# Kernel optimization log

Hardware: AMD Instinct MI355X
Metric: run time of the kernel (lower is better)

Reference implementation:

```python
import jax, jax.numpy as jnp
import numpy as np

N = 50000   # nodes
E = 800000  # edges
IN = 128
H = 256
OUT = 10
G = 128     # graphs in batch


def _uniform(key, shape, fan_in):
    bound = 1.0 / np.sqrt(fan_in)
    return jax.random.uniform(key, shape, jnp.float32, -bound, bound)


def setup_inputs() -> dict:
    key = jax.random.key(0)
    ks = jax.random.split(key, 12)
    x = jax.random.normal(ks[0], (N, IN), jnp.float32)
    edge_index = jax.random.randint(ks[1], (2, E), 0, N, dtype=jnp.int64)
    edge_weight = jax.random.uniform(ks[2], (E,), jnp.float32)
    batch = jnp.sort(jax.random.randint(ks[3], (N,), 0, G, dtype=jnp.int64))
    # GCNConv weights (bias=False)
    W0 = _uniform(ks[4], (IN, H), IN)
    W1 = _uniform(ks[5], (H, H), H)
    W2 = _uniform(ks[6], (H, H), H)
    # MLP head: [H, H, OUT]
    Wm1 = _uniform(ks[7], (H, H), H)
    bm1 = _uniform(ks[8], (H,), H)
    Wm2 = _uniform(ks[9], (H, OUT), H)
    bm2 = _uniform(ks[10], (OUT,), H)
    return dict(x=x, edge_index=edge_index, edge_weight=edge_weight, batch=batch,
                W0=W0, W1=W1, W2=W2, Wm1=Wm1, bm1=bm1, Wm2=Wm2, bm2=bm2)


def _gcn_conv(h, W, row, col, dinv_sqrt):
    """GCNConv with self-loops and symmetric deg^-1/2 normalization, bias=False.
    Self-loop contribution handled analytically (norm = dinv_sqrt[i]^2)."""
    hw = h @ W                                        # [N, H]
    norm = dinv_sqrt[row] * dinv_sqrt[col]            # [E]
    msg = hw[row] * norm[:, None]                     # [E, H] gather-scale
    agg = jax.ops.segment_sum(msg, col, num_segments=N)  # scatter-add at targets
    return agg + (dinv_sqrt * dinv_sqrt)[:, None] * hw    # add self-loop term


def reference(x, edge_index, edge_weight, batch, W0, W1, W2, Wm1, bm1, Wm2, bm2):
    row, col = edge_index[0], edge_index[1]
    # degree including self-loop (edge_weight is ignored, as in the source)
    deg = jax.ops.segment_sum(jnp.ones((E,), x.dtype), col, num_segments=N) + 1.0
    dinv_sqrt = jax.lax.rsqrt(deg)
    h = x
    for W in (W0, W1, W2):
        h = jax.nn.relu(_gcn_conv(h, W, row, col, dinv_sqrt))
    # global mean pool over graphs
    counts = jax.ops.segment_sum(jnp.ones((N,), h.dtype), batch, num_segments=G)
    pooled = jax.ops.segment_sum(h, batch, num_segments=G) / jnp.maximum(counts, 1.0)[:, None]
    # MLP head (dropout inactive at inference)
    hmid = jax.nn.relu(pooled @ Wm1 + bm1)
    last = hmid @ Wm2 + bm2
    return jax.nn.log_softmax(last, axis=-1), jax.nn.sigmoid(last), last
```

## Files before the change

### kernel.cpp

```cpp
#include <hip/hip_runtime.h>
#include <math.h>

#define N_NODES 50000
#define N_PAD   50048
#define N_EDGES 800000
#define CSR_CAP 1200000
#define IN_F 128
#define H_F 256
#define OUT_F 10
#define N_G 128
#define NCHUNKS 196

typedef __attribute__((ext_vector_type(4))) float f32x4;
typedef __attribute__((ext_vector_type(2))) float f32x2;
typedef unsigned char u8;

__device__ inline f32x2 fp8x2_f32_lo(unsigned int v) {
    return __builtin_amdgcn_cvt_pk_f32_fp8(v, false);
}
__device__ inline f32x2 fp8x2_f32_hi(unsigned int v) {
    return __builtin_amdgcn_cvt_pk_f32_fp8(v, true);
}
__device__ inline unsigned int f32_fp8x2_lo(float a, float b, unsigned int old) {
    return __builtin_amdgcn_cvt_pk_fp8_f32(a, b, old, false);
}
__device__ inline unsigned int f32_fp8x2_hi(float a, float b, unsigned int old) {
    return __builtin_amdgcn_cvt_pk_fp8_f32(a, b, old, true);
}
__device__ inline u8 f32_fp8(float a) {
    return (u8)(f32_fp8x2_lo(a, a, 0u) & 0xff);
}
__device__ inline ushort f2bf(float x) {
    union { float f; unsigned int u; } v; v.f = x;
    unsigned int r = v.u + 0x7fff + ((v.u >> 16) & 1);
    return (ushort)(r >> 16);
}
__device__ inline float bf2f(ushort u) {
    union { unsigned int u; float f; } v; v.u = ((unsigned int)u) << 16; return v.f;
}

__device__ inline void gl2lds16(const void* g, void* l) {
    __builtin_amdgcn_global_load_lds(
        (const __attribute__((address_space(1))) unsigned int*)g,
        (__attribute__((address_space(3))) unsigned int*)l,
        16, 0, 0);
}

#define PREP_HIST 782
#define PREP_X   (PREP_HIST + 6250)
#define PREP_T0  (PREP_X + 128)
#define PREP_T1  (PREP_T0 + 256)
#define PREP_T2  (PREP_T1 + 256)
#define PREP_GS  (PREP_T2 + NCHUNKS)

__global__ __launch_bounds__(256) void prep_kernel(
    const int* __restrict__ col, int* __restrict__ counts,
    int* __restrict__ rank,
    const float* __restrict__ x, u8* __restrict__ xb,
    const float* __restrict__ W0, u8* __restrict__ W0t,
    const float* __restrict__ W1, u8* __restrict__ W1t,
    const float* __restrict__ W2, u8* __restrict__ W2t,
    const int* __restrict__ batch, int* __restrict__ gstart) {
    int b = blockIdx.x;
    int tid = threadIdx.x;
    if (b < PREP_HIST) {
        int base = b * 1024 + tid;
        int c[4];
        #pragma unroll
        for (int u = 0; u < 4; ++u) {
            int e = base + u * 256;
            c[u] = (e < N_EDGES) ? col[e] : -1;
        }
        int rk[4];
        #pragma unroll
        for (int u = 0; u < 4; ++u)
            if (c[u] >= 0) rk[u] = atomicAdd(&counts[c[u]], 1);
        #pragma unroll
        for (int u = 0; u < 4; ++u)
            if (c[u] >= 0) rank[base + u * 256] = rk[u];
    } else if (b < PREP_X) {
        int i = (b - PREP_HIST) * 256 + tid;
        float4 v = *(const float4*)(x + (size_t)i * 4);
        unsigned int p = f32_fp8x2_lo(v.x, v.y, 0u);
        p = f32_fp8x2_hi(v.z, v.w, p);
        *(unsigned int*)(xb + (size_t)i * 4) = p;
    } else if (b < PREP_T0) {
        int idx = (b - PREP_X) * 256 + tid;
        int k = idx >> 8, nn = idx & 255;
        W0t[nn * IN_F + k] = f32_fp8(W0[idx]);
    } else if (b < PREP_T1) {
        int idx = (b - PREP_T0) * 256 + tid;
        int k = idx >> 8, nn = idx & 255;
        W1t[nn * H_F + k] = f32_fp8(W1[idx]);
    } else if (b < PREP_T2) {
        int idx = (b - PREP_T1) * 256 + tid;
        int k = idx >> 8, nn = idx & 255;
        W2t[nn * H_F + k] = f32_fp8(W2[idx]);
    } else {
        int i = (b - PREP_T2) * 256 + tid;
        if (i >= N_NODES) return;
        int bb = batch[i];
        if (i == 0) {
            for (int g = 0; g <= bb; ++g) gstart[g] = 0;
        } else {
            int p = batch[i - 1];
            if (p != bb) { for (int g = p + 1; g <= bb; ++g) gstart[g] = i; }
        }
        if (i == N_NODES - 1) {
            for (int g = bb + 1; g <= N_G; ++g) gstart[g] = N_NODES;
        }
    }
}

__global__ __launch_bounds__(256) void chunk_reduce(const int* __restrict__ counts,
                                                    int* __restrict__ csum, int n) {
    int i = blockIdx.x * 256 + threadIdx.x;
    int v = (i < n) ? ((counts[i] + 7) & ~7) : 0;
    #pragma unroll
    for (int off = 32; off; off >>= 1) v += __shfl_down(v, off);
    __shared__ int ws[4];
    if ((threadIdx.x & 63) == 0) ws[threadIdx.x >> 6] = v;
    __syncthreads();
    if (threadIdx.x == 0) csum[blockIdx.x] = ws[0] + ws[1] + ws[2] + ws[3];
}

__global__ __launch_bounds__(256) void scan_dinv_kernel(const int* __restrict__ counts,
                                                        const int* __restrict__ csum,
                                                        int* __restrict__ offsets,
                                                        float* __restrict__ dinv,
                                                        unsigned int* __restrict__ csr_ew,
                                                        int n) {
    int tid = threadIdx.x;
    int lane = tid & 63, wid = tid >> 6;
    int cv = (tid < NCHUNKS) ? csum[tid] : 0;
    int xc = cv;
    #pragma unroll
    for (int off = 1; off < 64; off <<= 1) {
        int t = __shfl_up(xc, off);
        if (lane >= off) xc += t;
    }
    __shared__ int cw[4], cpre[4];
    __shared__ int cexcl[257];
    if (lane == 63) cw[wid] = xc;
    __syncthreads();
    if (tid == 0) { int s = 0; for (int k = 0; k < 4; ++k) { cpre[k] = s; s += cw[k]; } }
    __syncthreads();
    cexcl[tid] = cpre[wid] + xc - cv;
    if (tid == 255) cexcl[256] = cpre[3] + cw[3];
    __syncthreads();
    int base = cexcl[blockIdx.x];
    int i = blockIdx.x * 256 + tid;
    int v = (i < n) ? counts[i] : 0;
    int pv = (v + 7) & ~7;
    int x = pv;
    #pragma unroll
    for (int off = 1; off < 64; off <<= 1) {
        int t = __shfl_up(x, off);
        if (lane >= off) x += t;
    }
    __shared__ int wsum[4], wpre[4];
    if (lane == 63) wsum[wid] = x;
    __syncthreads();
    if (tid == 0) { int s = 0; for (int k = 0; k < 4; ++k) { wpre[k] = s; s += wsum[k]; } }
    __syncthreads();
    if (i < n) {
        int o = base + wpre[wid] + x - pv;
        offsets[i] = o;
        dinv[i] = rsqrtf((float)(v + 1));
        for (int z = v; z < pv; ++z) csr_ew[o + z] = 0u;
    }
    if (blockIdx.x == 0 && tid == 0) offsets[n] = cexcl[NCHUNKS];
}

__global__ __launch_bounds__(256) void fill_csr_kernel(const int* __restrict__ row,
                                                       const int* __restrict__ col,
                                                       const int* __restrict__ offsets,
                                                       const int* __restrict__ rank,
                                                       const float* __restrict__ dinv,
                                                       unsigned int* __restrict__ csr_ew) {
    int e0 = blockIdx.x * 512 + threadIdx.x;
    int e1 = e0 + 256;
    int c0 = -1, c1 = -1, r0 = 0, r1 = 0, k0 = 0, k1 = 0;
    if (e0 < N_EDGES) { c0 = col[e0]; r0 = row[e0]; k0 = rank[e0]; }
    if (e1 < N_EDGES) { c1 = col[e1]; r1 = row[e1]; k1 = rank[e1]; }
    float dc0 = 0.f, dr0 = 0.f, dc1 = 0.f, dr1 = 0.f;
    if (c0 >= 0) { dc0 = dinv[c0]; dr0 = dinv[r0]; }
    if (c1 >= 0) { dc1 = dinv[c1]; dr1 = dinv[r1]; }
    if (c0 >= 0)
        csr_ew[offsets[c0] + k0] = (unsigned int)r0 | ((unsigned int)f2bf(dc0 * dr0) << 16);
    if (c1 >= 0)
        csr_ew[offsets[c1] + k1] = (unsigned int)r1 | ((unsigned int)f2bf(dc1 * dr1) << 16);
}

template <int K, bool RELU>
__global__ __launch_bounds__(256) void gemm_fp8(const u8* __restrict__ A,
                                                const u8* __restrict__ Bt,
                                                u8* __restrict__ C) {
    __shared__ u8 As[4 * 4096];
    __shared__ u8 Bs[4 * 4096];
    int tid = threadIdx.x;
    int lane = tid & 63;
    int w = tid >> 6;
    int wm = w & 1, wn = w >> 1;
    int l16 = lane & 15, quad = lane >> 4;
    int row0 = blockIdx.x * 128;
    int col0 = blockIdx.y * 128;
    f32x4 acc[4][4] = {};

    int sr = tid >> 1;
    int sh = (tid & 1) * 16;
    const u8* ga = A + (size_t)(row0 + sr) * K + sh;
    const u8* gb = Bt + (size_t)(col0 + sr) * K + sh;

    #pragma unroll
    for (int k0 = 0; k0 < K; k0 += 128) {
        if (k0) __syncthreads();
        #pragma unroll
        for (int q = 0; q < 4; ++q) {
            gl2lds16(ga + k0 + q * 32, As + q * 4096 + w * 1024);
            gl2lds16(gb + k0 + q * 32, Bs + q * 4096 + w * 1024);
        }
        __syncthreads();
        #pragma unroll
        for (int h = 0; h < 4; ++h) {
            long af[4], bfr[4];
            #pragma unroll
            for (int i = 0; i < 4; ++i)
                af[i] = *(const long*)&As[h * 4096 + (wm * 64 + i * 16 + l16) * 32 + quad * 8];
            #pragma unroll
            for (int j = 0; j < 4; ++j)
                bfr[j] = *(const long*)&Bs[h * 4096 + (wn * 64 + j * 16 + l16) * 32 + quad * 8];
            #pragma unroll
            for (int i = 0; i < 4; ++i)
                #pragma unroll
                for (int j = 0; j < 4; ++j)
                    acc[i][j] = __builtin_amdgcn_mfma_f32_16x16x32_fp8_fp8(af[i], bfr[j], acc[i][j], 0, 0, 0);
        }
    }
    #pragma unroll
    for (int i = 0; i < 4; ++i) {
        int rowb = row0 + wm * 64 + i * 16 + quad * 4;
        #pragma unroll
        for (int r = 0; r < 4; ++r) {
            int grow = rowb + r;
            #pragma unroll
            for (int j = 0; j < 4; ++j) {
                int gcol = col0 + wn * 64 + j * 16 + l16;
                float v = acc[i][j][r];
                if (RELU) v = fmaxf(v, 0.f);
                C[(size_t)grow * H_F + gcol] = f32_fp8(v);
            }
        }
    }
}

__global__ __launch_bounds__(256) void aggregate128(const u8* __restrict__ hw,
                                                    const float* __restrict__ dinv,
                                                    const int* __restrict__ offsets,
                                                    const unsigned int* __restrict__ csr_ew,
                                                    u8* __restrict__ hout) {
    int w = threadIdx.x >> 6;
    int lane = threadIdx.x & 63;
    int i = blockIdx.x * 4 + w;
    if (i >= N_NODES) return;
    float di = dinv[i];
    const u8* base = hw + (size_t)lane * 2;
    unsigned int su = *(const unsigned short*)(base + (size_t)i * IN_F);
    f32x2 sv = fp8x2_f32_lo(su);
    float s = di * di;
    float a0 = s * sv.x, a1 = s * sv.y;
    int t = __builtin_amdgcn_readfirstlane(offsets[i]);
    int end = __builtin_amdgcn_readfirstlane(offsets[i + 1]);
    if (t < end) {
        uint4 eA = *(const uint4*)(csr_ew + t);
        uint4 eB = *(const uint4*)(csr_ew + t + 4);
        for (; t < end; t += 8) {
            uint4 nA, nB;
            if (t + 8 < end) {
                nA = *(const uint4*)(csr_ew + t + 8);
                nB = *(const uint4*)(csr_ew + t + 12);
            }
            unsigned int e[8] = {eA.x, eA.y, eA.z, eA.w, eB.x, eB.y, eB.z, eB.w};
            unsigned int v[8];
            #pragma unroll
            for (int u = 0; u < 8; ++u)
                v[u] = *(const unsigned short*)(base + (size_t)(e[u] & 0xffff) * IN_F);
            #pragma unroll
            for (int u = 0; u < 8; ++u) {
                float wq = bf2f((ushort)(e[u] >> 16));
                f32x2 f = fp8x2_f32_lo(v[u]);
                a0 += wq * f.x; a1 += wq * f.y;
            }
            eA = nA; eB = nB;
        }
    }
    unsigned int o = f32_fp8x2_lo(a0, a1, 0u);
    *(unsigned short*)(hout + (size_t)i * IN_F + lane * 2) = (unsigned short)(o & 0xffff);
}

__global__ __launch_bounds__(256) void aggregate256(const u8* __restrict__ hw,
                                                    const float* __restrict__ dinv,
                                                    const int* __restrict__ offsets,
                                                    const unsigned int* __restrict__ csr_ew,
                                                    u8* __restrict__ hout) {
    int w = threadIdx.x >> 6;
    int lane = threadIdx.x & 63;
    int i = blockIdx.x * 4 + w;
    if (i >= N_NODES) return;
    float di = dinv[i];
    const u8* base = hw + (size_t)lane * 4;
    unsigned int su = *(const unsigned int*)(base + (size_t)i * H_F);
    f32x2 slo = fp8x2_f32_lo(su), shi = fp8x2_f32_hi(su);
    float s = di * di;
    float a0 = s * slo.x, a1 = s * slo.y, a2 = s * shi.x, a3 = s * shi.y;
    int t = __builtin_amdgcn_readfirstlane(offsets[i]);
    int end = __builtin_amdgcn_readfirstlane(offsets[i + 1]);
    if (t < end) {
        uint4 eA = *(const uint4*)(csr_ew + t);
        uint4 eB = *(const uint4*)(csr_ew + t + 4);
        for (; t < end; t += 8) {
            uint4 nA, nB;
            if (t + 8 < end) {
                nA = *(const uint4*)(csr_ew + t + 8);
                nB = *(const uint4*)(csr_ew + t + 12);
            }
            unsigned int e[8] = {eA.x, eA.y, eA.z, eA.w, eB.x, eB.y, eB.z, eB.w};
            unsigned int v[8];
            #pragma unroll
            for (int u = 0; u < 8; ++u)
                v[u] = *(const unsigned int*)(base + (size_t)(e[u] & 0xffff) * H_F);
            #pragma unroll
            for (int u = 0; u < 8; ++u) {
                float wq = bf2f((ushort)(e[u] >> 16));
                f32x2 lo = fp8x2_f32_lo(v[u]), hi = fp8x2_f32_hi(v[u]);
                a0 += wq * lo.x; a1 += wq * lo.y;
                a2 += wq * hi.x; a3 += wq * hi.y;
            }
            eA = nA; eB = nB;
        }
    }
    unsigned int o = f32_fp8x2_lo(fmaxf(a0, 0.f), fmaxf(a1, 0.f), 0u);
    o = f32_fp8x2_hi(fmaxf(a2, 0.f), fmaxf(a3, 0.f), o);
    *(unsigned int*)(hout + (size_t)i * H_F + lane * 4) = o;
}

__global__ __launch_bounds__(1024) void pool_mlp_kernel(const u8* __restrict__ h,
                                                        const int* __restrict__ gstart,
                                                        const float* __restrict__ Wm1,
                                                        const float* __restrict__ bm1,
                                                        const float* __restrict__ Wm2,
                                                        const float* __restrict__ bm2,
                                                        float* __restrict__ out) {
    __shared__ float sm[16][H_F];
    __shared__ float p[H_F];
    __shared__ float hmid[H_F];
    __shared__ float lastv[OUT_F];
    __shared__ float stats[2];
    int g = blockIdx.x;
    int s = gstart[g], e = gstart[g + 1];
    int w = threadIdx.x >> 6;
    int lane = threadIdx.x & 63;
    float a0 = 0.f, a1 = 0.f, a2 = 0.f, a3 = 0.f;
    for (int i = s + w; i < e; i += 16) {
        unsigned int v = *(const unsigned int*)(h + (size_t)i * H_F + lane * 4);
        f32x2 lo = fp8x2_f32_lo(v), hi = fp8x2_f32_hi(v);
        a0 += lo.x; a1 += lo.y; a2 += hi.x; a3 += hi.y;
    }
    *(f32x4*)&sm[w][lane * 4] = (f32x4){a0, a1, a2, a3};
    __syncthreads();
    int j = threadIdx.x;
    int cnt = e - s;
    if (j < H_F) {
        float t = 0.f;
        #pragma unroll
        for (int k = 0; k < 16; ++k) t += sm[k][j];
        p[j] = t / (float)max(cnt, 1);
    }
    __syncthreads();
    if (j < H_F) {
        float acc = bm1[j];
        for (int k = 0; k < H_F; ++k) acc += p[k] * Wm1[k * H_F + j];
        hmid[j] = fmaxf(acc, 0.f);
    }
    __syncthreads();
    if (j < OUT_F) {
        float a = bm2[j];
        for (int k = 0; k < H_F; ++k) a += hmid[k] * Wm2[k * OUT_F + j];
        lastv[j] = a;
    }
    __syncthreads();
    if (j == 0) {
        float m = -1e30f;
        for (int o = 0; o < OUT_F; ++o) m = fmaxf(m, lastv[o]);
        float sxp = 0.f;
        for (int o = 0; o < OUT_F; ++o) sxp += expf(lastv[o] - m);
        stats[0] = m; stats[1] = logf(sxp);
    }
    __syncthreads();
    if (j < OUT_F) {
        float v = lastv[j];
        out[g * OUT_F + j] = v - stats[0] - stats[1];
        out[(size_t)N_G * OUT_F + g * OUT_F + j] = 1.f / (1.f + expf(-v));
        out[(size_t)2 * N_G * OUT_F + g * OUT_F + j] = v;
    }
}

extern "C" void kernel_launch(void* const* d_in, const int* in_sizes, int n_in,
                              void* d_out, int out_size, void* d_ws, size_t ws_size,
                              hipStream_t stream) {
    const float* x   = (const float*)d_in[0];
    const int* edge_index = (const int*)d_in[1];
    const int* batch = (const int*)d_in[3];
    const float* W0  = (const float*)d_in[4];
    const float* W1  = (const float*)d_in[5];
    const float* W2  = (const float*)d_in[6];
    const float* Wm1 = (const float*)d_in[7];
    const float* bm1 = (const float*)d_in[8];
    const float* Wm2 = (const float*)d_in[9];
    const float* bm2 = (const float*)d_in[10];
    float* out = (float*)d_out;

    char* ws = (char*)d_ws;
    size_t off = 0;
    auto alloc = [&](size_t bytes) -> void* {
        void* p = ws + off; off += (bytes + 255) & ~(size_t)255; return p;
    };
    u8* xb       = (u8*)alloc((size_t)N_PAD * IN_F);
    u8* bufA     = (u8*)alloc((size_t)N_PAD * H_F);
    u8* bufB     = (u8*)alloc((size_t)N_PAD * H_F);
    u8* t0       = (u8*)alloc((size_t)N_PAD * IN_F);
    u8* W0t      = (u8*)alloc((size_t)H_F * IN_F);
    u8* W1t      = (u8*)alloc((size_t)H_F * H_F);
    u8* W2t      = (u8*)alloc((size_t)H_F * H_F);
    float* dinv    = (float*)alloc((size_t)N_NODES * 4);
    int*   counts  = (int*)alloc((size_t)N_NODES * 4);
    int*   offsets = (int*)alloc((size_t)(N_NODES + 1) * 4);
    int*   rank    = (int*)alloc((size_t)N_EDGES * 4);
    unsigned int* csr_ew = (unsigned int*)alloc((size_t)CSR_CAP * 4);
    int*   csum    = (int*)alloc((size_t)256 * 4);
    int*   gstart  = (int*)alloc((size_t)(N_G + 1) * 4);

    const int* row = edge_index;
    const int* col = edge_index + N_EDGES;

    hipMemsetAsync(counts, 0, (size_t)N_NODES * 4, stream);

    prep_kernel<<<PREP_GS, 256, 0, stream>>>(col, counts, rank, x, xb, W0, W0t,
                                             W1, W1t, W2, W2t, batch, gstart);
    chunk_reduce<<<NCHUNKS, 256, 0, stream>>>(counts, csum, N_NODES);
    scan_dinv_kernel<<<NCHUNKS, 256, 0, stream>>>(counts, csum, offsets, dinv,
                                                  csr_ew, N_NODES);
    fill_csr_kernel<<<1563, 256, 0, stream>>>(row, col, offsets, rank, dinv, csr_ew);

    dim3 gg(N_PAD / 128, H_F / 128);
    int agg_blocks = (N_NODES + 3) / 4;
    aggregate128<<<agg_blocks, 256, 0, stream>>>(xb, dinv, offsets, csr_ew, t0);
    gemm_fp8<IN_F, true><<<gg, 256, 0, stream>>>(t0, W0t, bufA);
    gemm_fp8<H_F, false><<<gg, 256, 0, stream>>>(bufA, W1t, bufB);
    aggregate256<<<agg_blocks, 256, 0, stream>>>(bufB, dinv, offsets, csr_ew, bufA);
    gemm_fp8<H_F, false><<<gg, 256, 0, stream>>>(bufA, W2t, bufB);
    aggregate256<<<agg_blocks, 256, 0, stream>>>(bufB, dinv, offsets, csr_ew, bufA);

    pool_mlp_kernel<<<N_G, 1024, 0, stream>>>(bufA, gstart, Wm1, bm1, Wm2, bm2, out);
}
```

Baseline: 290.9 us.

## Replace global atomic degree histogram with partitioned LDS histograms

Swaps the global-atomic degree histogram for a 16x16 grid of blocks. Each block scans one edge partition and counts in LDS only the edges whose targets fall in its node range. Per-partition counts are summed in chunk_reduce and turned into per-partition exclusive offsets in scan_dinv, and fill_csr adds that offset to the LDS rank. This removes global atomic contention and the memset, but each edge is now read 16 times by the histogram blocks, and only 256 blocks each loop over 50k edges.

```diff
diff --git a/kernel.cpp b/kernel.cpp
--- a/kernel.cpp
+++ b/kernel.cpp
@@ -11,6 +11,11 @@
 #define N_G 128
 #define NCHUNKS 196
 
+#define P_PART 16
+#define R_RANGE 16
+#define PE (N_EDGES / P_PART)
+#define RN (N_NODES / R_RANGE)
+
 typedef __attribute__((ext_vector_type(4))) float f32x4;
 typedef __attribute__((ext_vector_type(2))) float f32x2;
 typedef unsigned char u8;
@@ -46,40 +51,43 @@
         16, 0, 0);
 }
 
-#define PREP_HIST 782
-#define PREP_X   (PREP_HIST + 6250)
+#define PREP_HB  (P_PART * R_RANGE)
+#define PREP_X   (PREP_HB + 6250)
 #define PREP_T0  (PREP_X + 128)
 #define PREP_T1  (PREP_T0 + 256)
 #define PREP_T2  (PREP_T1 + 256)
 #define PREP_GS  (PREP_T2 + NCHUNKS)
 
 __global__ __launch_bounds__(256) void prep_kernel(
-    const int* __restrict__ col, int* __restrict__ counts,
+    const int* __restrict__ col, int* __restrict__ H,
     int* __restrict__ rank,
     const float* __restrict__ x, u8* __restrict__ xb,
     const float* __restrict__ W0, u8* __restrict__ W0t,
     const float* __restrict__ W1, u8* __restrict__ W1t,
     const float* __restrict__ W2, u8* __restrict__ W2t,
     const int* __restrict__ batch, int* __restrict__ gstart) {
+    __shared__ int hcnt[RN];
     int b = blockIdx.x;
     int tid = threadIdx.x;
-    if (b < PREP_HIST) {
-        int base = b * 1024 + tid;
-        int c[4];
-        #pragma unroll
-        for (int u = 0; u < 4; ++u) {
-            int e = base + u * 256;
-            c[u] = (e < N_EDGES) ? col[e] : -1;
-        }
-        int rk[4];
-        #pragma unroll
-        for (int u = 0; u < 4; ++u)
-            if (c[u] >= 0) rk[u] = atomicAdd(&counts[c[u]], 1);
-        #pragma unroll
-        for (int u = 0; u < 4; ++u)
-            if (c[u] >= 0) rank[base + u * 256] = rk[u];
+    if (b < PREP_HB) {
+        int p = b & (P_PART - 1);
+        int r = b >> 4;
+        for (int j = tid; j < RN; j += 256) hcnt[j] = 0;
+        __syncthreads();
+        int nb = r * RN;
+        int e0 = p * PE;
+        for (int e = e0 + tid; e < e0 + PE; e += 256) {
+            int c = col[e];
+            unsigned int d = (unsigned int)(c - nb);
+            if (d < RN) {
+                int lr = atomicAdd(&hcnt[d], 1);
+                rank[e] = lr;
+            }
+        }
+        __syncthreads();
+        for (int j = tid; j < RN; j += 256) H[p * N_NODES + nb + j] = hcnt[j];
     } else if (b < PREP_X) {
-        int i = (b - PREP_HIST) * 256 + tid;
+        int i = (b - PREP_HB) * 256 + tid;
         float4 v = *(const float4*)(x + (size_t)i * 4);
         unsigned int p = f32_fp8x2_lo(v.x, v.y, 0u);
         p = f32_fp8x2_hi(v.z, v.w, p);
@@ -112,10 +120,17 @@
     }
 }
 
-__global__ __launch_bounds__(256) void chunk_reduce(const int* __restrict__ counts,
+__global__ __launch_bounds__(256) void chunk_reduce(const int* __restrict__ H,
+                                                    int* __restrict__ counts,
                                                     int* __restrict__ csum, int n) {
     int i = blockIdx.x * 256 + threadIdx.x;
-    int v = (i < n) ? ((counts[i] + 7) & ~7) : 0;
+    int total = 0;
+    if (i < n) {
+        #pragma unroll
+        for (int p = 0; p < P_PART; ++p) total += H[p * N_NODES + i];
+        counts[i] = total;
+    }
+    int v = (i < n) ? ((total + 7) & ~7) : 0;
     #pragma unroll
     for (int off = 32; off; off >>= 1) v += __shfl_down(v, off);
     __shared__ int ws[4];
@@ -127,6 +142,7 @@
 __global__ __launch_bounds__(256) void scan_dinv_kernel(const int* __restrict__ counts,
                                                         const int* __restrict__ csum,
                                                         int* __restrict__ offsets,
+                                                        int* __restrict__ H,
                                                         float* __restrict__ dinv,
                                                         unsigned int* __restrict__ csr_ew,
                                                         int n) {
@@ -168,6 +184,13 @@
         offsets[i] = o;
         dinv[i] = rsqrtf((float)(v + 1));
         for (int z = v; z < pv; ++z) csr_ew[o + z] = 0u;
+        int s = 0;
+        #pragma unroll
+        for (int p = 0; p < P_PART; ++p) {
+            int hv = H[p * N_NODES + i];
+            H[p * N_NODES + i] = s;
+            s += hv;
+        }
     }
     if (blockIdx.x == 0 && tid == 0) offsets[n] = cexcl[NCHUNKS];
 }
@@ -175,6 +198,7 @@
 __global__ __launch_bounds__(256) void fill_csr_kernel(const int* __restrict__ row,
                                                        const int* __restrict__ col,
                                                        const int* __restrict__ offsets,
+                                                       const int* __restrict__ H,
                                                        const int* __restrict__ rank,
                                                        const float* __restrict__ dinv,
                                                        unsigned int* __restrict__ csr_ew) {
@@ -184,12 +208,19 @@
     if (e0 < N_EDGES) { c0 = col[e0]; r0 = row[e0]; k0 = rank[e0]; }
     if (e1 < N_EDGES) { c1 = col[e1]; r1 = row[e1]; k1 = rank[e1]; }
     float dc0 = 0.f, dr0 = 0.f, dc1 = 0.f, dr1 = 0.f;
-    if (c0 >= 0) { dc0 = dinv[c0]; dr0 = dinv[r0]; }
-    if (c1 >= 0) { dc1 = dinv[c1]; dr1 = dinv[r1]; }
+    int h0 = 0, h1 = 0;
+    if (c0 >= 0) {
+        dc0 = dinv[c0]; dr0 = dinv[r0];
+        h0 = H[(e0 / PE) * N_NODES + c0];
+    }
+    if (c1 >= 0) {
+        dc1 = dinv[c1]; dr1 = dinv[r1];
+        h1 = H[(e1 / PE) * N_NODES + c1];
+    }
     if (c0 >= 0)
-        csr_ew[offsets[c0] + k0] = (unsigned int)r0 | ((unsigned int)f2bf(dc0 * dr0) << 16);
+        csr_ew[offsets[c0] + h0 + k0] = (unsigned int)r0 | ((unsigned int)f2bf(dc0 * dr0) << 16);
     if (c1 >= 0)
-        csr_ew[offsets[c1] + k1] = (unsigned int)r1 | ((unsigned int)f2bf(dc1 * dr1) << 16);
+        csr_ew[offsets[c1] + h1 + k1] = (unsigned int)r1 | ((unsigned int)f2bf(dc1 * dr1) << 16);
 }
 
 template <int K, bool RELU>
@@ -436,6 +467,7 @@
     int*   counts  = (int*)alloc((size_t)N_NODES * 4);
     int*   offsets = (int*)alloc((size_t)(N_NODES + 1) * 4);
     int*   rank    = (int*)alloc((size_t)N_EDGES * 4);
+    int*   H       = (int*)alloc((size_t)P_PART * N_NODES * 4);
     unsigned int* csr_ew = (unsigned int*)alloc((size_t)CSR_CAP * 4);
     int*   csum    = (int*)alloc((size_t)256 * 4);
     int*   gstart  = (int*)alloc((size_t)(N_G + 1) * 4);
@@ -443,14 +475,12 @@
     const int* row = edge_index;
     const int* col = edge_index + N_EDGES;
 
-    hipMemsetAsync(counts, 0, (size_t)N_NODES * 4, stream);
-
-    prep_kernel<<<PREP_GS, 256, 0, stream>>>(col, counts, rank, x, xb, W0, W0t,
+    prep_kernel<<<PREP_GS, 256, 0, stream>>>(col, H, rank, x, xb, W0, W0t,
                                              W1, W1t, W2, W2t, batch, gstart);
-    chunk_reduce<<<NCHUNKS, 256, 0, stream>>>(counts, csum, N_NODES);
-    scan_dinv_kernel<<<NCHUNKS, 256, 0, stream>>>(counts, csum, offsets, dinv,
+    chunk_reduce<<<NCHUNKS, 256, 0, stream>>>(H, counts, csum, N_NODES);
+    scan_dinv_kernel<<<NCHUNKS, 256, 0, stream>>>(counts, csum, offsets, H, dinv,
                                                   csr_ew, N_NODES);
-    fill_csr_kernel<<<1563, 256, 0, stream>>>(row, col, offsets, rank, dinv, csr_ew);
+    fill_csr_kernel<<<1563, 256, 0, stream>>>(row, col, offsets, H, rank, dinv, csr_ew);
 
     dim3 gg(N_PAD / 128, H_F / 128);
     int agg_blocks = (N_NODES + 3) / 4;
```

Measured after the change: 315.5 us. +8.5%, slower.
